# Kernel tuning notes

Measured on AMD Instinct MI355X. Metric: run time of the kernel, lower is better.

## Reference

```python
import math
import jax, jax.numpy as jnp
import numpy as np

B, T, E = 2, 2048, 2048
NUM_HEADS = 16
H = NUM_HEADS // 2          # differential head pairs = 8
D = E // NUM_HEADS          # head_dim = 128
DEPTH = 12
LAMBDA_INIT = 0.8 - 0.6 * math.exp(-0.3 * DEPTH)
EPS = 1e-5


def setup_inputs() -> dict:
    key = jax.random.key(0)
    ks = jax.random.split(key, 10)
    sc = lambda k, shape, std: jax.random.normal(k, shape, dtype=jnp.float32) * std
    return {
        "x": jax.random.normal(ks[0], (B, T, E), dtype=jnp.float32),
        "Wq": sc(ks[1], (E, E), 0.02),   # [in, out]
        "Wk": sc(ks[2], (E, E), 0.02),   # n_rep == 1 -> k/v proj width = embed_dim
        "Wv": sc(ks[3], (E, E), 0.02),
        "Wo": sc(ks[4], (E, E), 0.02),
        "lambda_q1": sc(ks[5], (D,), 0.1),
        "lambda_k1": sc(ks[6], (D,), 0.1),
        "lambda_q2": sc(ks[7], (D,), 0.1),
        "lambda_k2": sc(ks[8], (D,), 0.1),
        "g": jnp.ones((2 * D,), dtype=jnp.float32),  # RMSNorm weight
    }


def _forward(x, Wq, Wk, Wv, Wo, lq1, lk1, lq2, lk2, g):
    Bz, Tl, _ = x.shape
    # projections; view(bsz, T, 2*H, D).reshape(bsz, T, H, 2, D): adjacent head
    # pairs become the two differential components.
    q = (x @ Wq).reshape(Bz, Tl, H, 2, D)
    k = (x @ Wk).reshape(Bz, Tl, H, 2, D)
    v = (x @ Wv).reshape(Bz, Tl, H, 2 * D)   # value width is 2*head_dim

    scale = D ** -0.5                         # SDPA default scaling
    causal = jnp.tril(jnp.ones((Tl, Tl), dtype=bool))  # is_causal=True

    def attend(qc, kc):
        # qc, kc: [B, T, H, D]
        s = jnp.einsum('bthd,bshd->bhts', qc, kc) * scale
        s = jnp.where(causal, s, -jnp.inf)
        a = jax.nn.softmax(s, axis=-1)
        return jnp.einsum('bhts,bshe->bthe', a, v)  # [B, T, H, 2D]

    # interleaved q/k + repeated v in the single SDPA == two attention maps on full V
    o1 = attend(q[..., 0, :], k[..., 0, :])
    o2 = attend(q[..., 1, :], k[..., 1, :])

    lam = jnp.exp(jnp.sum(lq1 * lk1)) - jnp.exp(jnp.sum(lq2 * lk2)) + LAMBDA_INIT
    o = o1 - lam * o2
    # RMSNorm over last dim (2*head_dim), eps=1e-5, learned weight g
    o = o * jax.lax.rsqrt(jnp.mean(o * o, axis=-1, keepdims=True) + EPS) * g
    o = o * (1.0 - LAMBDA_INIT)
    return o.reshape(Bz, Tl, E) @ Wo


def reference(x, Wq, Wk, Wv, Wo, lambda_q1, lambda_k1, lambda_q2, lambda_k2, g):
    return _forward(x, Wq, Wk, Wv, Wo, lambda_q1, lambda_k1, lambda_q2, lambda_k2, g)
```

## Files before the change

### kernel.cpp

```cpp
#include <hip/hip_runtime.h>
#include <stdint.h>
#include <math.h>


typedef unsigned short u16;
typedef short bf16x8 __attribute__((ext_vector_type(8)));
typedef float f32x4 __attribute__((ext_vector_type(4)));

typedef uint32_t __attribute__((address_space(1))) as1_u32;
typedef uint32_t __attribute__((address_space(3))) as3_u32;

#define LAMBDA_INIT 0.78360576653162453f

__device__ __forceinline__ u16 f2bf(float f) {
  uint32_t u = __float_as_uint(f);
  u += 0x7FFFu + ((u >> 16) & 1u);
  return (u16)(u >> 16);
}
__device__ __forceinline__ float bf2f(u16 v) {
  return __uint_as_float(((uint32_t)v) << 16);
}

__device__ __forceinline__ void async16(u16* lds, const u16* g) {
  __builtin_amdgcn_global_load_lds((const as1_u32*)(uintptr_t)g,
                                   (as3_u32*)(uint32_t)(uintptr_t)lds, 16, 0, 0);
}

__device__ __forceinline__ f32x4 mfma16(bf16x8 a, bf16x8 b, f32x4 c) {
  return __builtin_amdgcn_mfma_f32_16x16x32_bf16(a, b, c, 0, 0, 0);
}


__global__ void cast_x_kernel(const float* __restrict__ x, u16* __restrict__ xb, int n4) {
  int i = blockIdx.x * 256 + threadIdx.x;
  if (i < n4) {
    float4 v = ((const float4*)x)[i];
    ushort4 o;
    o.x = f2bf(v.x); o.y = f2bf(v.y); o.z = f2bf(v.z); o.w = f2bf(v.w);
    ((ushort4*)xb)[i] = o;
  }
}

__global__ void transpose_w4_kernel(const float* __restrict__ W0, const float* __restrict__ W1,
                                    const float* __restrict__ W2, const float* __restrict__ W3,
                                    u16* __restrict__ Wt4) {
  __shared__ float tile[32][33];
  int z = blockIdx.z;
  const float* W = (z == 0) ? W0 : (z == 1) ? W1 : (z == 2) ? W2 : W3;
  u16* Wt = Wt4 + (size_t)z * 4194304;
  int tx = threadIdx.x, ty = threadIdx.y;
  int c0 = blockIdx.x * 32, r0 = blockIdx.y * 32;
#pragma unroll
  for (int i = 0; i < 32; i += 8)
    tile[ty + i][tx] = W[(size_t)(r0 + ty + i) * 2048 + c0 + tx];
  __syncthreads();
#pragma unroll
  for (int i = 0; i < 32; i += 8)
    Wt[(size_t)(c0 + ty + i) * 2048 + r0 + tx] = f2bf(tile[tx][ty + i]);
}

__global__ void lam_kernel(const float* __restrict__ lq1, const float* __restrict__ lk1,
                           const float* __restrict__ lq2, const float* __restrict__ lk2,
                           float* __restrict__ out) {
  int L = threadIdx.x;
  float d1 = lq1[L] * lk1[L] + lq1[L + 64] * lk1[L + 64];
  float d2 = lq2[L] * lk2[L] + lq2[L + 64] * lk2[L + 64];
#pragma unroll
  for (int m = 1; m < 64; m <<= 1) {
    d1 += __shfl_xor(d1, m);
    d2 += __shfl_xor(d2, m);
  }
  if (L == 0) out[0] = __expf(d1) - __expf(d2) + LAMBDA_INIT;
}

template <int OUT_BF16>
__global__ __launch_bounds__(256, 3) void gemm_bt_kernel(const u16* __restrict__ A,
                                                         const u16* __restrict__ Bt,
                                                         void* __restrict__ Cout,
                                                         int M, int N, int K) {
  __shared__ __attribute__((aligned(16))) u16 As[128 * 64];
  __shared__ __attribute__((aligned(16))) u16 Bs[128 * 64];
  int t = threadIdx.x;
  int lane = t & 63, w = t >> 6;
  int lr = lane & 15, lq = lane >> 4;
  int m0 = blockIdx.y * 128, n0 = blockIdx.x * 128;
  int wm = (w >> 1) * 64, wn = (w & 1) * 64;
  const u16* Ab = A + (size_t)m0 * K;
  const u16* Bb = Bt + (size_t)n0 * K;
  f32x4 acc[4][4] = {};

  for (int k0 = 0; k0 < K; k0 += 64) {
    __syncthreads();
#pragma unroll
    for (int i = 0; i < 4; i++) {
      int q = t + i * 256;
      int row = q >> 3, gp = q & 7;
      int gg = gp ^ (row & 7);
      async16(&As[q * 8], Ab + (size_t)row * K + k0 + gg * 8);
      async16(&Bs[q * 8], Bb + (size_t)row * K + k0 + gg * 8);
    }
    __syncthreads();
#pragma unroll
    for (int kk = 0; kk < 2; kk++) {
      bf16x8 a[4], b[4];
#pragma unroll
      for (int mi = 0; mi < 4; mi++) {
        int ra = wm + mi * 16 + lr;
        int rb = wn + mi * 16 + lr;
        a[mi] = *(const bf16x8*)&As[ra * 64 + ((kk * 4 + lq) ^ (ra & 7)) * 8];
        b[mi] = *(const bf16x8*)&Bs[rb * 64 + ((kk * 4 + lq) ^ (rb & 7)) * 8];
      }
#pragma unroll
      for (int mi = 0; mi < 4; mi++)
#pragma unroll
        for (int ni = 0; ni < 4; ni++)
          acc[mi][ni] = mfma16(a[mi], b[ni], acc[mi][ni]);
    }
  }
#pragma unroll
  for (int mi = 0; mi < 4; mi++) {
#pragma unroll
    for (int ni = 0; ni < 4; ni++) {
#pragma unroll
      for (int r = 0; r < 4; r++) {
        int row = m0 + wm + mi * 16 + lq * 4 + r;
        int col = n0 + wn + ni * 16 + lr;
        if (OUT_BF16)
          ((u16*)Cout)[(size_t)row * N + col] = f2bf(acc[mi][ni][r]);
        else
          ((float*)Cout)[(size_t)row * N + col] = acc[mi][ni][r];
      }
    }
  }
}


struct FlashCtx {
  const u16* Qbase;
  const u16* Kbase;
  const u16* Vbase;
  int t, w, lr, lq;
};

__device__ __forceinline__ void stage_k(const FlashCtx& cx, int jc, u16* Kn) {
#pragma unroll
  for (int i = 0; i < 4; i++) {
    int q = cx.t + i * 256;
    int row = q >> 4, gp = q & 15;
    int gg = (gp & 8) | ((gp & 7) ^ (row & 7));
    async16(&Kn[q * 8], cx.Kbase + (size_t)(jc + row) * 4096 + gg * 8);
  }
}

__device__ __forceinline__ void stage_v(const FlashCtx& cx, int jc, u16* Vs) {
#pragma unroll
  for (int i = 0; i < 8; i++) {
    int q = cx.t + i * 256;
    int e = q >> 3, gp = q & 7;
    int gg = gp ^ (e & 7);
    async16(&Vs[q * 8], cx.Vbase + (size_t)e * 4096 + jc + gg * 8);
  }
}

__global__ __launch_bounds__(256, 2) void flash_diff_kernel(const u16* __restrict__ QKb,
                                                            const u16* __restrict__ Vt,
                                                            u16* __restrict__ o12b) {
  __shared__ __attribute__((aligned(16))) u16 Ks0[64 * 128];
  __shared__ __attribute__((aligned(16))) u16 Ks1[64 * 128];
  __shared__ __attribute__((aligned(16))) u16 Vs[256 * 64];
  __shared__ __attribute__((aligned(16))) u16 Ps[4][16 * 88];

  int t = threadIdx.x;
  FlashCtx cx;
  cx.t = t; cx.w = t >> 6;
  cx.lr = t & 15; cx.lq = (t >> 4) & 3;

  int idx = blockIdx.x;
  int xcd = idx & 7, slot = idx >> 3;
  int pairI = slot & 15, ghi = slot >> 4;
  int g = ghi * 8 + xcd;
  int bh = g >> 1, c = g & 1;
  int b = bh >> 3, h = bh & 7;

  cx.Qbase = QKb + (size_t)b * 2048 * 4096 + h * 256 + c * 128;
  cx.Kbase = cx.Qbase + 2048;
  cx.Vbase = Vt + (size_t)(h * 256) * 4096 + b * 2048;
  u16* Op = o12b + (size_t)c * (4096ull * 2048) + (size_t)b * 2048 * 2048 + h * 256;
  u16* PsW = Ps[cx.w];

  u16* Kc = Ks0;
  u16* Kn = Ks1;

  stage_k(cx, 0, Kc);

#pragma unroll 1
  for (int phase = 0; phase < 2; phase++) {
    int qi = phase ? (31 - pairI) : pairI;
    int q0 = qi * 64;
    int nst = qi + 1;

    bf16x8 qa[4];
#pragma unroll
    for (int ks = 0; ks < 4; ks++)
      qa[ks] = *(const bf16x8*)&cx.Qbase[(size_t)(q0 + cx.w * 16 + cx.lr) * 4096 +
                                         ks * 32 + cx.lq * 8];

    f32x4 acc[16] = {};
    f32x4 lacc = {};
    float m_ = -INFINITY;
    int rowmax = q0 + cx.w * 16 + 15;

#pragma unroll 1
    for (int j = 0; j < nst; j++) {
      int jc = j * 64;
      int njc = (j + 1 < nst) ? (j + 1) * 64 : (phase == 0 ? 0 : -1);

      __syncthreads();
      if (njc >= 0) stage_k(cx, njc, Kn);
      stage_v(cx, jc, Vs);

      bool act = (jc <= rowmax);
      if (act) {
        f32x4 sacc[4] = {};
#pragma unroll
        for (int ks = 0; ks < 4; ks++) {
#pragma unroll
          for (int ni = 0; ni < 4; ni++) {
            int row = ni * 16 + cx.lr;
            int gk = ks * 4 + cx.lq;
            int gp = (gk & 8) | ((gk & 7) ^ (row & 7));
            bf16x8 kb = *(const bf16x8*)&Kc[row * 128 + gp * 8];
            sacc[ni] = mfma16(qa[ks], kb, sacc[ni]);
          }
        }

        const float k2 = 0.12753257550036097f;
        float s2[4][4];
        bool diag = (jc + 63 > q0 + cx.w * 16);
#pragma unroll
        for (int ni = 0; ni < 4; ni++)
#pragma unroll
          for (int r = 0; r < 4; r++) {
            float v = sacc[ni][r] * k2;
            if (diag) {
              int colg = jc + ni * 16 + cx.lr;
              int rowg = q0 + cx.w * 16 + cx.lq * 4 + r;
              if (colg > rowg) v = -INFINITY;
            }
            s2[ni][r] = v;
          }

        float sm = fmaxf(
            fmaxf(fmaxf(fmaxf(s2[0][0], s2[0][1]), fmaxf(s2[0][2], s2[0][3])),
                  fmaxf(fmaxf(s2[1][0], s2[1][1]), fmaxf(s2[1][2], s2[1][3]))),
            fmaxf(fmaxf(fmaxf(s2[2][0], s2[2][1]), fmaxf(s2[2][2], s2[2][3])),
                  fmaxf(fmaxf(s2[3][0], s2[3][1]), fmaxf(s2[3][2], s2[3][3]))));
        float mo = m_;
        if (__any(sm > mo + 8.0f)) {
          float mv = sm;
          mv = fmaxf(mv, __shfl_xor(mv, 1));
          mv = fmaxf(mv, __shfl_xor(mv, 2));
          mv = fmaxf(mv, __shfl_xor(mv, 4));
          mv = fmaxf(mv, __shfl_xor(mv, 8));
          mv = fmaxf(mv, __shfl_xor(mv, 16));
          mv = fmaxf(mv, __shfl_xor(mv, 32));
          float mn = fmaxf(mo, mv);
          float a = __builtin_amdgcn_exp2f(mo - mn);
#pragma unroll
          for (int ei = 0; ei < 16; ei++)
#pragma unroll
            for (int r = 0; r < 4; r++) acc[ei][r] *= a;
#pragma unroll
          for (int r = 0; r < 4; r++) lacc[r] *= a;
          m_ = mn;
          mo = mn;
        }

#pragma unroll
        for (int ni = 0; ni < 4; ni++)
#pragma unroll
          for (int r = 0; r < 4; r++) {
            float p = __builtin_amdgcn_exp2f(s2[ni][r] - mo);
            PsW[(cx.lq * 4 + r) * 88 + ni * 16 + cx.lr] =
                (u16)(__float_as_uint(p) >> 16);
          }
      }

      __syncthreads();
      if (act) {
        const bf16x8 onesb = {0x3F80, 0x3F80, 0x3F80, 0x3F80,
                              0x3F80, 0x3F80, 0x3F80, 0x3F80};
        bf16x8 pa0 = *(const bf16x8*)&PsW[cx.lr * 88 + cx.lq * 8];
        bf16x8 pa1 = *(const bf16x8*)&PsW[cx.lr * 88 + 32 + cx.lq * 8];
        __builtin_amdgcn_s_setprio(1);
#pragma unroll
        for (int ei = 0; ei < 16; ei++) {
          int e = ei * 16 + cx.lr;
          int g0 = cx.lq ^ (e & 7);
          int g1 = g0 ^ 4;
          bf16x8 vb0 = *(const bf16x8*)&Vs[e * 64 + g0 * 8];
          bf16x8 vb1 = *(const bf16x8*)&Vs[e * 64 + g1 * 8];
          acc[ei] = mfma16(pa0, vb0, acc[ei]);
          acc[ei] = mfma16(pa1, vb1, acc[ei]);
        }
        lacc = mfma16(pa0, onesb, lacc);
        lacc = mfma16(pa1, onesb, lacc);
        __builtin_amdgcn_s_setprio(0);
      }

      u16* tmp = Kc; Kc = Kn; Kn = tmp;
    }

#pragma unroll
    for (int r = 0; r < 4; r++) {
      float inv = 1.0f / lacc[r];
      int row = q0 + cx.w * 16 + cx.lq * 4 + r;
#pragma unroll
      for (int ei = 0; ei < 16; ei++)
        Op[(size_t)row * 2048 + ei * 16 + cx.lr] = f2bf(acc[ei][r] * inv);
    }
  }
}

__global__ void combine_kernel(const u16* __restrict__ o12b, const float* __restrict__ lamp,
                               const float* __restrict__ g, u16* __restrict__ ob) {
  __shared__ float red[4];
  int t = threadIdx.x;
  int grp = blockIdx.x;
  size_t idx = (size_t)grp * 256 + t;
  const size_t comp = 4096ull * 2048;
  float lam = lamp[0];
  float v = bf2f(o12b[idx]) - lam * bf2f(o12b[idx + comp]);
  float ss = v * v;
  ss += __shfl_xor(ss, 1);
  ss += __shfl_xor(ss, 2);
  ss += __shfl_xor(ss, 4);
  ss += __shfl_xor(ss, 8);
  ss += __shfl_xor(ss, 16);
  ss += __shfl_xor(ss, 32);
  if ((t & 63) == 0) red[t >> 6] = ss;
  __syncthreads();
  float tot = red[0] + red[1] + red[2] + red[3];
  float scale = rsqrtf(tot * (1.0f / 256.0f) + 1e-5f) * (1.0f - LAMBDA_INIT);
  ob[(size_t)(grp >> 3) * 2048 + (grp & 7) * 256 + t] = f2bf(v * scale * g[t]);
}


extern "C" void kernel_launch(void* const* d_in, const int* in_sizes, int n_in,
                              void* d_out, int out_size, void* d_ws, size_t ws_size,
                              hipStream_t stream) {
  const float* x   = (const float*)d_in[0];
  const float* Wq  = (const float*)d_in[1];
  const float* Wk  = (const float*)d_in[2];
  const float* Wv  = (const float*)d_in[3];
  const float* Wo  = (const float*)d_in[4];
  const float* lq1 = (const float*)d_in[5];
  const float* lk1 = (const float*)d_in[6];
  const float* lq2 = (const float*)d_in[7];
  const float* lk2 = (const float*)d_in[8];
  const float* g   = (const float*)d_in[9];

  char* ws = (char*)d_ws;
  u16* xb    = (u16*)(ws);
  u16* Wtq   = (u16*)(ws + 16777216);
  u16* Wtv   = (u16*)(ws + 33554432);
  u16* Wto   = (u16*)(ws + 41943040);
  u16* QKb   = (u16*)(ws + 50331648);
  u16* Vt    = (u16*)(ws + 83886080);
  u16* o12b  = (u16*)(ws + 100663296);
  u16* ob    = (u16*)(ws + 134217728);
  float* lamp = (float*)(ws + 150994944);

  cast_x_kernel<<<8192, 256, 0, stream>>>(x, xb, 2097152);
  transpose_w4_kernel<<<dim3(64, 64, 4), dim3(32, 8), 0, stream>>>(Wq, Wk, Wv, Wo, Wtq);
  lam_kernel<<<1, 64, 0, stream>>>(lq1, lk1, lq2, lk2, lamp);

  gemm_bt_kernel<1><<<dim3(32, 32), 256, 0, stream>>>(xb, Wtq, QKb, 4096, 4096, 2048);
  gemm_bt_kernel<1><<<dim3(32, 16), 256, 0, stream>>>(Wtv, xb, Vt, 2048, 4096, 2048);

  flash_diff_kernel<<<512, 256, 0, stream>>>(QKb, Vt, o12b);
  combine_kernel<<<32768, 256, 0, stream>>>(o12b, lamp, g, ob);
  gemm_bt_kernel<0><<<dim3(16, 32), 256, 0, stream>>>(ob, Wto, (float*)d_out, 4096, 2048, 2048);
}
```

Baseline: 403.6 us.

## Add 256x256 multi-stage pipelined GEMM for QK projection; relax flash-attn V barrier

Adds a new 512-thread GEMM with 256x256 output tiles, a 4-buffer LDS ring fed by async global-to-LDS loads three steps ahead, swizzled LDS reads and fine-grained vmcnt waits, and uses it for the fused Q/K projection. The goal is more data reuse per tile and hiding global load latency behind MFMA work. In the flash attention kernel, V staging is issued before K staging and the full syncthreads is replaced by a partial vmcnt wait plus barrier, so the next K prefetch can stay in flight during P·V. The trade-off is higher register and LDS pressure and a grid of only 256 blocks on the big GEMM.

```diff
diff --git a/kernel.cpp b/kernel.cpp
--- a/kernel.cpp
+++ b/kernel.cpp
@@ -71,6 +71,104 @@
     d2 += __shfl_xor(d2, m);
   }
   if (L == 0) out[0] = __expf(d1) - __expf(d2) + LAMBDA_INIT;
+}
+
+
+__device__ __forceinline__ void stage256(const u16* base, int K, int k0, u16* lds, int t_) {
+#pragma unroll
+  for (int i = 0; i < 2; i++) {
+    int s = t_ + i * 512;
+    int row = s >> 2, gp = s & 3;
+    int gs = gp ^ ((row >> 1) & 3);
+    async16(&lds[s * 8], base + (size_t)row * K + k0 + gs * 8);
+  }
+}
+
+__global__ __launch_bounds__(512, 2) void gemm256_kernel(const u16* __restrict__ A,
+                                                         const u16* __restrict__ Bt,
+                                                         u16* __restrict__ Cout,
+                                                         int M, int N, int K) {
+  __shared__ __attribute__((aligned(16))) u16 Ls[4][2][256 * 32];
+  int t_ = threadIdx.x;
+  int lane = t_ & 63, w = t_ >> 6;
+  int lr = lane & 15, lq = lane >> 4;
+  int m0 = blockIdx.y * 256, n0 = blockIdx.x * 256;
+  int wm = (w >> 2) * 128, wn = (w & 3) * 64;
+  const u16* Ab = A + (size_t)m0 * K;
+  const u16* Bb = Bt + (size_t)n0 * K;
+  int NT = K >> 5;
+  f32x4 acc[8][4] = {};
+
+#pragma unroll
+  for (int p = 0; p < 3; p++) {
+    stage256(Ab, K, p * 32, &Ls[p][0][0], t_);
+    stage256(Bb, K, p * 32, &Ls[p][1][0], t_);
+  }
+  asm volatile("s_waitcnt vmcnt(8)" ::: "memory");
+  __builtin_amdgcn_s_barrier();
+  __builtin_amdgcn_sched_barrier(0);
+
+#pragma unroll 1
+  for (int t = 0; t < NT; t++) {
+    int d = t & 3;
+    const u16* As_ = &Ls[d][0][0];
+    const u16* Bs_ = &Ls[d][1][0];
+    bool stg = (t + 3 < NT);
+    int k0n = (t + 3) * 32;
+    int dn = (t + 3) & 3;
+
+    bf16x8 b4[4], a0[4];
+#pragma unroll
+    for (int nf = 0; nf < 4; nf++) {
+      int rb = wn + nf * 16 + lr;
+      b4[nf] = *(const bf16x8*)&Bs_[rb * 32 + (lq ^ ((rb >> 1) & 3)) * 8];
+    }
+#pragma unroll
+    for (int mf = 0; mf < 4; mf++) {
+      int ra = wm + mf * 16 + lr;
+      a0[mf] = *(const bf16x8*)&As_[ra * 32 + (lq ^ ((ra >> 1) & 3)) * 8];
+    }
+    if (stg) stage256(Ab, K, k0n, &Ls[dn][0][0], t_);
+    __builtin_amdgcn_s_setprio(1);
+#pragma unroll
+    for (int mf = 0; mf < 4; mf++)
+#pragma unroll
+      for (int nf = 0; nf < 4; nf++)
+        acc[mf][nf] = mfma16(a0[mf], b4[nf], acc[mf][nf]);
+    __builtin_amdgcn_s_setprio(0);
+
+    bf16x8 a1[4];
+#pragma unroll
+    for (int mf = 0; mf < 4; mf++) {
+      int ra = wm + 64 + mf * 16 + lr;
+      a1[mf] = *(const bf16x8*)&As_[ra * 32 + (lq ^ ((ra >> 1) & 3)) * 8];
+    }
+    if (stg) stage256(Bb, K, k0n, &Ls[dn][1][0], t_);
+    __builtin_amdgcn_s_setprio(1);
+#pragma unroll
+    for (int mf = 0; mf < 4; mf++)
+#pragma unroll
+      for (int nf = 0; nf < 4; nf++)
+        acc[4 + mf][nf] = mfma16(a1[mf], b4[nf], acc[4 + mf][nf]);
+    __builtin_amdgcn_s_setprio(0);
+
+    if (t < NT - 3)      asm volatile("s_waitcnt vmcnt(8)" ::: "memory");
+    else if (t < NT - 2) asm volatile("s_waitcnt vmcnt(4)" ::: "memory");
+    else                 asm volatile("s_waitcnt vmcnt(0)" ::: "memory");
+    __builtin_amdgcn_s_barrier();
+    __builtin_amdgcn_sched_barrier(0);
+  }
+
+#pragma unroll
+  for (int mf = 0; mf < 8; mf++)
+#pragma unroll
+    for (int nf = 0; nf < 4; nf++)
+#pragma unroll
+      for (int r = 0; r < 4; r++) {
+        int row = m0 + wm + mf * 16 + lq * 4 + r;
+        int col = n0 + wn + nf * 16 + lr;
+        Cout[(size_t)row * N + col] = f2bf(acc[mf][nf][r]);
+      }
 }
 
 template <int OUT_BF16>
@@ -216,8 +314,8 @@
       int njc = (j + 1 < nst) ? (j + 1) * 64 : (phase == 0 ? 0 : -1);
 
       __syncthreads();
+      stage_v(cx, jc, Vs);
       if (njc >= 0) stage_k(cx, njc, Kn);
-      stage_v(cx, jc, Vs);
 
       bool act = (jc <= rowmax);
       if (act) {
@@ -286,7 +384,11 @@
           }
       }
 
-      __syncthreads();
+      if (njc >= 0) asm volatile("s_waitcnt vmcnt(4)" ::: "memory");
+      else          asm volatile("s_waitcnt vmcnt(0)" ::: "memory");
+      __builtin_amdgcn_s_barrier();
+      __builtin_amdgcn_sched_barrier(0);
+
       if (act) {
         const bf16x8 onesb = {0x3F80, 0x3F80, 0x3F80, 0x3F80,
                               0x3F80, 0x3F80, 0x3F80, 0x3F80};
@@ -375,7 +477,7 @@
   transpose_w4_kernel<<<dim3(64, 64, 4), dim3(32, 8), 0, stream>>>(Wq, Wk, Wv, Wo, Wtq);
   lam_kernel<<<1, 64, 0, stream>>>(lq1, lk1, lq2, lk2, lamp);
 
-  gemm_bt_kernel<1><<<dim3(32, 32), 256, 0, stream>>>(xb, Wtq, QKb, 4096, 4096, 2048);
+  gemm256_kernel<<<dim3(16, 16), 512, 0, stream>>>(xb, Wtq, QKb, 4096, 4096, 2048);
   gemm_bt_kernel<1><<<dim3(32, 16), 256, 0, stream>>>(Wtv, xb, Vt, 2048, 4096, 2048);
 
   flash_diff_kernel<<<512, 256, 0, stream>>>(QKb, Vt, o12b);
```

Result: no change. 398.3 us (-1.3%).
